# Kernel tuning notes

Hardware: AMD Instinct MI355X
Metric: run time of the kernel (lower is better)

Reference implementation:

```python
import jax, jax.numpy as jnp
import numpy as np

DIM = 768
HEADS = 12
HEAD_DIM = DIM // HEADS
HIDDEN = 4 * DIM
EPS = 1e-5
SCALE = HEAD_DIM ** -0.5


def _ln(x, g, b):
    mu = jnp.mean(x, axis=-1, keepdims=True)
    var = jnp.var(x, axis=-1, keepdims=True)
    return (x - mu) * jax.lax.rsqrt(var + EPS) * g + b


def setup_inputs() -> dict:
    key = jax.random.key(0)
    ks = jax.random.split(key, 10)
    s = lambda fan_in: 1.0 / np.sqrt(fan_in)
    return {
        "x": jax.random.normal(ks[0], (8, 4, 512, DIM), dtype=jnp.float32),
        "g1": jnp.ones((DIM,), jnp.float32),
        "b1": jnp.zeros((DIM,), jnp.float32),
        "Wqkv": jax.random.normal(ks[1], (DIM, 3 * DIM), jnp.float32) * s(DIM),
        "Wp": jax.random.normal(ks[2], (DIM, DIM), jnp.float32) * s(DIM),
        "bp": jnp.zeros((DIM,), jnp.float32),
        "g2": jnp.ones((DIM,), jnp.float32),
        "b2": jnp.zeros((DIM,), jnp.float32),
        "W1": jax.random.normal(ks[3], (DIM, HIDDEN), jnp.float32) * s(DIM),
        "bm1": jnp.zeros((HIDDEN,), jnp.float32),
        "W2": jax.random.normal(ks[4], (HIDDEN, DIM), jnp.float32) * s(HIDDEN),
        "bm2": jnp.zeros((DIM,), jnp.float32),
    }


def reference(x, g1, b1, Wqkv, Wp, bp, g2, b2, W1, bm1, W2, bm2):
    B, S, N, D = x.shape
    h = _ln(x, g1, b1)
    qkv = h @ Wqkv                                   # [B,S,N,3D]
    qkv = qkv.reshape(B, S, N, 3, HEADS, HEAD_DIM)
    q, k, v = (qkv[..., i, :, :] for i in range(3))  # [B,S,N,H,Dh]
    # scores over tokens N, per head
    attn = jnp.einsum("bsnhd,bsmhd->bshnm", q, k) * SCALE
    attn = jax.nn.softmax(attn, axis=-1)
    y = jnp.einsum("bshnm,bsmhd->bsnhd", attn, v).reshape(B, S, N, D)
    y = y @ Wp + bp
    x = x + y
    h2 = _ln(x, g2, b2)
    m = jax.nn.gelu(h2 @ W1 + bm1, approximate=False) @ W2 + bm2
    return x + m
```

## Files before the change

### kernel.cpp

```cpp
#include <hip/hip_runtime.h>
#include <hip/hip_bf16.h>
#include <cstdint>


typedef __bf16 bf16;
typedef bf16 bf16x8 __attribute__((ext_vector_type(8)));
typedef float f32x4 __attribute__((ext_vector_type(4)));
typedef uint32_t u32;

__device__ __forceinline__ f32x4 mfma16(bf16x8 a, bf16x8 b, f32x4 c){
  return __builtin_amdgcn_mfma_f32_16x16x32_bf16(a, b, c, 0, 0, 0);
}

__device__ __forceinline__ void gload16(const void* g, const void* l){
  __builtin_amdgcn_global_load_lds(
      (__attribute__((address_space(1))) u32*)(uintptr_t)g,
      (__attribute__((address_space(3))) u32*)(u32)(uintptr_t)l,
      16, 0, 0);
}

__global__ __launch_bounds__(256)
void transpose_cast(const float* __restrict__ W, bf16* __restrict__ Wt, int K, int N)
{
  __shared__ float t[64][65];
  int n0 = blockIdx.x * 64, k0 = blockIdx.y * 64;
  int tid = threadIdx.x;
  int c = tid & 63, r4 = tid >> 6;
#pragma unroll
  for (int i = 0; i < 16; ++i){
    int r = r4 * 16 + i;
    t[r][c] = W[(size_t)(k0 + r) * N + n0 + c];
  }
  __syncthreads();
#pragma unroll
  for (int i = 0; i < 16; ++i){
    int r = r4 * 16 + i;
    Wt[(size_t)(n0 + r) * K + k0 + c] = (bf16)t[c][r];
  }
}

__global__ __launch_bounds__(256)
void ln_kernel(const float* __restrict__ x, const float* __restrict__ g,
               const float* __restrict__ b, bf16* __restrict__ out)
{
  int row = blockIdx.x;
  int tid = threadIdx.x;
  const float* xr = x + (size_t)row * 768;
  float v0 = xr[tid], v1 = xr[tid + 256], v2 = xr[tid + 512];
  float s = v0 + v1 + v2;
  float ss = v0*v0 + v1*v1 + v2*v2;
#pragma unroll
  for (int m = 1; m < 64; m <<= 1){
    s  += __shfl_xor(s,  m, 64);
    ss += __shfl_xor(ss, m, 64);
  }
  __shared__ float red[8];
  int w = tid >> 6, l = tid & 63;
  if (l == 0){ red[w] = s; red[4 + w] = ss; }
  __syncthreads();
  s  = red[0] + red[1] + red[2] + red[3];
  ss = red[4] + red[5] + red[6] + red[7];
  float mu  = s * (1.0f / 768.0f);
  float var = ss * (1.0f / 768.0f) - mu * mu;
  float rs  = rsqrtf(var + 1e-5f);
  bf16* o = out + (size_t)row * 768;
  o[tid]       = (bf16)((v0 - mu) * rs * g[tid]       + b[tid]);
  o[tid + 256] = (bf16)((v1 - mu) * rs * g[tid + 256] + b[tid + 256]);
  o[tid + 512] = (bf16)((v2 - mu) * rs * g[tid + 512] + b[tid + 512]);
}

template<int EPI>
__global__ __launch_bounds__(512, 2)
void gemm256(const bf16* __restrict__ A, const bf16* __restrict__ Bt,
             const float* __restrict__ bias, const float* __restrict__ res,
             void* __restrict__ Cout, int M, int N, int K)
{
  extern __shared__ bf16 lds[];
  const int tid = threadIdx.x;
  const int w = tid >> 6, l = tid & 63;
  const int lr = l & 15, lg = l >> 4;
  const int wr = w >> 2, wc = w & 3;
  const int nbm = M >> 8, nbn = N >> 8;
  const int nwg = nbm * nbn;
  const int cpx = nwg >> 3;
  const int bid = (int)blockIdx.x;
  const int sw  = (bid & 7) * cpx + (bid >> 3);
  const int bm = sw % nbm, bn = sw / nbm;
  const int rowA0 = bm << 8, colB0 = bn << 8;

  f32x4 acc[8][4];
#pragma unroll
  for (int i = 0; i < 8; ++i)
#pragma unroll
    for (int j = 0; j < 4; ++j) acc[i][j] = f32x4{0.f, 0.f, 0.f, 0.f};

  const int srow = l >> 3;
  const int sg   = (l & 7) ^ srow;
  auto stA = [&](int T, int q){
    bf16* dst = lds + (size_t)(T & 1) * 32768 + q * 4096 + w * 512;
    int row = q * 64 + w * 8 + srow;
    gload16(A + (size_t)(rowA0 + row) * K + T * 64 + sg * 8, dst);
  };
  auto stB = [&](int T, int nh, int j){
    int hh = j * 8 + w;
    int row0 = (hh >> 2) * 64 + nh * 32 + (hh & 3) * 8;
    bf16* dst = lds + (size_t)(T & 1) * 32768 + 16384 + row0 * 64;
    int row = row0 + srow;
    gload16(Bt + (size_t)(colB0 + row) * K + T * 64 + sg * 8, dst);
  };

  const int NT = K >> 6;

  stA(0,0); stA(0,2); stB(0,0,0); stB(0,0,1);
  stA(0,1); stA(0,3); stB(0,1,0); stB(0,1,1);
  asm volatile("s_waitcnt vmcnt(4)" ::: "memory");
  __builtin_amdgcn_s_barrier();

#define PHASE(MH, NH, STAGE_STMT)                                              \
  {                                                                            \
    bf16x8 af[4][2], bfr[2][2];                                                \
    _Pragma("unroll")                                                          \
    for (int fr = 0; fr < 4; ++fr)                                             \
      _Pragma("unroll")                                                        \
      for (int kk = 0; kk < 2; ++kk){                                          \
        int row = wr * 128 + (MH) * 64 + fr * 16 + lr;                         \
        af[fr][kk] = *(const bf16x8*)&Abuf[row * 64 +                          \
                       (((kk * 4 + lg) ^ (lr & 7)) << 3)];                     \
      }                                                                        \
    _Pragma("unroll")                                                          \
    for (int fc = 0; fc < 2; ++fc)                                             \
      _Pragma("unroll")                                                        \
      for (int kk = 0; kk < 2; ++kk){                                          \
        int row = wc * 64 + (NH) * 32 + fc * 16 + lr;                          \
        bfr[fc][kk] = *(const bf16x8*)&Bbuf[row * 64 +                         \
                       (((kk * 4 + lg) ^ (lr & 7)) << 3)];                     \
      }                                                                        \
    STAGE_STMT;                                                                \
    if (more) asm volatile("s_waitcnt vmcnt(4)" ::: "memory");                 \
    else      asm volatile("s_waitcnt vmcnt(0)" ::: "memory");                 \
    __builtin_amdgcn_s_barrier();                                              \
    __builtin_amdgcn_s_setprio(1);                                             \
    _Pragma("unroll")                                                          \
    for (int fr = 0; fr < 4; ++fr)                                             \
      _Pragma("unroll")                                                        \
      for (int fc = 0; fc < 2; ++fc)                                           \
        _Pragma("unroll")                                                      \
        for (int kk = 0; kk < 2; ++kk)                                         \
          acc[(MH) * 4 + fr][(NH) * 2 + fc] =                                  \
              mfma16(af[fr][kk], bfr[fc][kk], acc[(MH) * 4 + fr][(NH) * 2 + fc]); \
    __builtin_amdgcn_s_setprio(0);                                             \
    __builtin_amdgcn_s_barrier();                                              \
  }

  for (int T = 0; T < NT; ++T){
    const bf16* Abuf = lds + (size_t)(T & 1) * 32768;
    const bf16* Bbuf = Abuf + 16384;
    const bool more = (T + 1 < NT);
    PHASE(0, 0, if (more){ stA(T+1,0); stA(T+1,2); })
    PHASE(1, 0, if (more){ stB(T+1,0,0); stB(T+1,0,1); })
    PHASE(0, 1, if (more){ stA(T+1,1); stA(T+1,3); })
    PHASE(1, 1, if (more){ stB(T+1,1,0); stB(T+1,1,1); })
  }
#undef PHASE

  const size_t crow = (size_t)rowA0 + wr * 128;
  const size_t ccol = (size_t)colB0 + wc * 64;
#pragma unroll
  for (int mi = 0; mi < 8; ++mi){
#pragma unroll
    for (int ni = 0; ni < 4; ++ni){
      size_t r0 = crow + (mi >> 2) * 64 + (mi & 3) * 16 + lg * 4;
      size_t c  = ccol + (ni >> 1) * 32 + (ni & 1) * 16 + lr;
#pragma unroll
      for (int i = 0; i < 4; ++i){
        size_t r = r0 + i;
        float v = acc[mi][ni][i];
        if (EPI == 0){
          ((bf16*)Cout)[r * (size_t)N + c] = (bf16)v;
        } else if (EPI == 1){
          v += bias[c];
          v = 0.5f * v * (1.0f + erff(v * 0.70710678118654752f));
          ((bf16*)Cout)[r * (size_t)N + c] = (bf16)v;
        } else {
          v += bias[c] + res[r * (size_t)N + c];
          ((float*)Cout)[r * (size_t)N + c] = v;
        }
      }
    }
  }
}

__global__ __launch_bounds__(256)
void attn_kernel(const bf16* __restrict__ qkv, bf16* __restrict__ y)
{
  int bid = blockIdx.x;
  int qt  = bid & 7;
  int bsh = bid >> 3;
  int h = bsh % 12;
  int R = bsh / 12;
  size_t rowbase = (size_t)R * 512;
  int tid = threadIdx.x, w = tid >> 6, l = tid & 63;
  int lr = l & 15, lg = l >> 4;

  __shared__ bf16 Kl[64 * 64];
  __shared__ bf16 Vt[64 * 64];
  __shared__ bf16 Pl[4][16 * 64];

  int q0 = qt * 64 + w * 16;
  bf16x8 qf[2];
#pragma unroll
  for (int ks = 0; ks < 2; ++ks)
    qf[ks] = *(const bf16x8*)&qkv[(rowbase + q0 + lr) * 2304 + h * 64 + ks * 32 + lg * 8];

  float mi[4], li[4];
  f32x4 oa[4];
#pragma unroll
  for (int i = 0; i < 4; ++i){ mi[i] = -1e30f; li[i] = 0.f; }
#pragma unroll
  for (int dt = 0; dt < 4; ++dt) oa[dt] = f32x4{0.f, 0.f, 0.f, 0.f};

  for (int c = 0; c < 8; ++c){
    __syncthreads();
    size_t tokbase = rowbase + c * 64;
#pragma unroll
    for (int it = 0; it < 2; ++it){
      int idx = it * 256 + tid;
      int t  = idx >> 3;
      int c8 = idx & 7;
      bf16x8 kv = *(const bf16x8*)&qkv[(tokbase + t) * 2304 + 768 + h * 64 + c8 * 8];
      *(bf16x8*)&Kl[t * 64 + ((c8 ^ (t & 7)) * 8)] = kv;
      bf16x8 vv = *(const bf16x8*)&qkv[(tokbase + t) * 2304 + 1536 + h * 64 + c8 * 8];
#pragma unroll
      for (int j = 0; j < 8; ++j){
        int d = c8 * 8 + j;
        Vt[d * 64 + (((t >> 3) ^ (d & 7)) * 8) + (t & 7)] = vv[j];
      }
    }
    __syncthreads();

    f32x4 s[4];
#pragma unroll
    for (int tt = 0; tt < 4; ++tt){
      f32x4 a = f32x4{0.f, 0.f, 0.f, 0.f};
#pragma unroll
      for (int ks = 0; ks < 2; ++ks){
        int row = tt * 16 + lr;
        int c8 = ks * 4 + lg;
        bf16x8 kf = *(const bf16x8*)&Kl[row * 64 + ((c8 ^ (row & 7)) * 8)];
        a = mfma16(qf[ks], kf, a);
      }
      s[tt] = a * 0.125f;
    }

    float pr[4][4];
#pragma unroll
    for (int i = 0; i < 4; ++i){
      float rm = fmaxf(fmaxf(s[0][i], s[1][i]), fmaxf(s[2][i], s[3][i]));
#pragma unroll
      for (int mm = 1; mm < 16; mm <<= 1) rm = fmaxf(rm, __shfl_xor(rm, mm, 64));
      float mn = fmaxf(mi[i], rm);
      float corr = __expf(mi[i] - mn);
      float rs = 0.f;
#pragma unroll
      for (int tt = 0; tt < 4; ++tt){
        float p = __expf(s[tt][i] - mn);
        pr[tt][i] = p;
        rs += p;
      }
#pragma unroll
      for (int mm = 1; mm < 16; mm <<= 1) rs += __shfl_xor(rs, mm, 64);
      li[i] = li[i] * corr + rs;
#pragma unroll
      for (int dt = 0; dt < 4; ++dt) oa[dt][i] *= corr;
      mi[i] = mn;
    }

#pragma unroll
    for (int i = 0; i < 4; ++i){
      int qr = lg * 4 + i;
#pragma unroll
      for (int tt = 0; tt < 4; ++tt){
        int tok = tt * 16 + lr;
        Pl[w][qr * 64 + (((tok >> 3) ^ (qr & 7)) * 8) + (tok & 7)] = (bf16)pr[tt][i];
      }
    }
    __syncthreads();

#pragma unroll
    for (int ks = 0; ks < 2; ++ks){
      bf16x8 pf = *(const bf16x8*)&Pl[w][lr * 64 + (((ks * 4 + lg) ^ (lr & 7)) * 8)];
#pragma unroll
      for (int dt = 0; dt < 4; ++dt){
        int row = dt * 16 + lr;
        int c8 = ks * 4 + lg;
        bf16x8 vf = *(const bf16x8*)&Vt[row * 64 + ((c8 ^ (row & 7)) * 8)];
        oa[dt] = mfma16(pf, vf, oa[dt]);
      }
    }
  }

#pragma unroll
  for (int i = 0; i < 4; ++i){
    float inv = 1.0f / li[i];
    size_t r = rowbase + q0 + lg * 4 + i;
#pragma unroll
    for (int dt = 0; dt < 4; ++dt)
      y[r * 768 + h * 64 + dt * 16 + lr] = (bf16)(oa[dt][i] * inv);
  }
}

extern "C" void kernel_launch(void* const* d_in, const int* in_sizes, int n_in,
                              void* d_out, int out_size, void* d_ws, size_t ws_size,
                              hipStream_t stream)
{
  (void)in_sizes; (void)n_in; (void)out_size; (void)ws_size;
  const float* x    = (const float*)d_in[0];
  const float* g1   = (const float*)d_in[1];
  const float* b1   = (const float*)d_in[2];
  const float* Wqkv = (const float*)d_in[3];
  const float* Wp   = (const float*)d_in[4];
  const float* bp   = (const float*)d_in[5];
  const float* g2   = (const float*)d_in[6];
  const float* b2   = (const float*)d_in[7];
  const float* W1   = (const float*)d_in[8];
  const float* bm1  = (const float*)d_in[9];
  const float* W2   = (const float*)d_in[10];
  const float* bm2  = (const float*)d_in[11];
  float* out = (float*)d_out;

  hipFuncSetAttribute((const void*)gemm256<0>, hipFuncAttributeMaxDynamicSharedMemorySize, 131072);
  hipFuncSetAttribute((const void*)gemm256<1>, hipFuncAttributeMaxDynamicSharedMemorySize, 131072);
  hipFuncSetAttribute((const void*)gemm256<2>, hipFuncAttributeMaxDynamicSharedMemorySize, 131072);

  char* ws = (char*)d_ws;
  size_t off = 0;
  auto alloc = [&](size_t nbytes) -> void* {
    void* p = ws + off;
    off += (nbytes + 255) & ~(size_t)255;
    return p;
  };
  bf16* WqkvT = (bf16*)alloc((size_t)2304 * 768 * 2);
  bf16* WpT   = (bf16*)alloc((size_t)768 * 768 * 2);
  bf16* W1T   = (bf16*)alloc((size_t)3072 * 768 * 2);
  bf16* W2T   = (bf16*)alloc((size_t)768 * 3072 * 2);
  char* R1 = (char*)alloc((size_t)16384 * 768 * 2);
  char* R2 = (char*)alloc((size_t)16384 * 3072 * 2);
  bf16* h   = (bf16*)R1;
  bf16* yb  = (bf16*)R1;
  bf16* h2  = (bf16*)R1;
  bf16* qkv = (bf16*)R2;
  bf16* m1  = (bf16*)R2;
  float* x2 = out;

  transpose_cast<<<dim3(36, 12), dim3(256), 0, stream>>>(Wqkv, WqkvT, 768, 2304);
  transpose_cast<<<dim3(12, 12), dim3(256), 0, stream>>>(Wp,   WpT,   768, 768);
  transpose_cast<<<dim3(48, 12), dim3(256), 0, stream>>>(W1,   W1T,   768, 3072);
  transpose_cast<<<dim3(12, 48), dim3(256), 0, stream>>>(W2,   W2T,   3072, 768);

  ln_kernel<<<dim3(16384), dim3(256), 0, stream>>>(x, g1, b1, h);
  gemm256<0><<<dim3(576), dim3(512), 131072, stream>>>(h, WqkvT, nullptr, nullptr,
                                                       (void*)qkv, 16384, 2304, 768);
  attn_kernel<<<dim3(3072), dim3(256), 0, stream>>>(qkv, yb);
  gemm256<2><<<dim3(192), dim3(512), 131072, stream>>>(yb, WpT, bp, x,
                                                       (void*)x2, 16384, 768, 768);
  ln_kernel<<<dim3(16384), dim3(256), 0, stream>>>(x2, g2, b2, h2);
  gemm256<1><<<dim3(768), dim3(512), 131072, stream>>>(h2, W1T, bm1, nullptr,
                                                       (void*)m1, 16384, 3072, 768);
  gemm256<2><<<dim3(192), dim3(512), 131072, stream>>>(m1, W2T, bm2, x2,
                                                       (void*)out, 16384, 768, 3072);
}
```

Baseline: 658.6 us.

## Use 128-row GEMM tiles for narrow-N projections and restructure K-loop phases

Templates the GEMM on the M-tile height so the two N=768 GEMMs (attention output projection and MLP down projection) use 128x256 tiles, doubling their workgroup count from 192 to 384 so more CUs are busy. The K-loop is rewritten to reuse A fragments across the two N halves and to keep both B halves in registers, with the staging and waitcnt sequence reorganised per tile shape. The block-to-tile mapping is also swapped to iterate N fastest. Smaller tiles lower per-block reuse and raise global traffic for those GEMMs, and the changed vmcnt accounting risks hazards if it is miscounted.

After: 686.3 us. 1.04x slower.

```diff
diff --git a/kernel.cpp b/kernel.cpp
--- a/kernel.cpp
+++ b/kernel.cpp
@@ -69,104 +69,147 @@
   o[tid + 512] = (bf16)((v2 - mu) * rs * g[tid + 512] + b[tid + 512]);
 }
 
-template<int EPI>
+template<int EPI, int BMQ>
 __global__ __launch_bounds__(512, 2)
 void gemm256(const bf16* __restrict__ A, const bf16* __restrict__ Bt,
              const float* __restrict__ bias, const float* __restrict__ res,
              void* __restrict__ Cout, int M, int N, int K)
 {
+  constexpr int BM   = BMQ * 64;
+  constexpr int MHN  = BMQ / 2;
+  constexpr int ABUF = BM * 64;
+  constexpr int BUFE = ABUF + 16384;
   extern __shared__ bf16 lds[];
   const int tid = threadIdx.x;
   const int w = tid >> 6, l = tid & 63;
   const int lr = l & 15, lg = l >> 4;
   const int wr = w >> 2, wc = w & 3;
-  const int nbm = M >> 8, nbn = N >> 8;
+  const int nbm = M / BM, nbn = N >> 8;
   const int nwg = nbm * nbn;
   const int cpx = nwg >> 3;
   const int bid = (int)blockIdx.x;
   const int sw  = (bid & 7) * cpx + (bid >> 3);
-  const int bm = sw % nbm, bn = sw / nbm;
-  const int rowA0 = bm << 8, colB0 = bn << 8;
-
-  f32x4 acc[8][4];
-#pragma unroll
-  for (int i = 0; i < 8; ++i)
+  const int bn = sw % nbn, bm = sw / nbn;
+  const int rowA0 = bm * BM, colB0 = bn << 8;
+
+  f32x4 acc[MHN * 4][4];
+#pragma unroll
+  for (int i = 0; i < MHN * 4; ++i)
 #pragma unroll
     for (int j = 0; j < 4; ++j) acc[i][j] = f32x4{0.f, 0.f, 0.f, 0.f};
 
   const int srow = l >> 3;
   const int sg   = (l & 7) ^ srow;
-  auto stA = [&](int T, int q){
-    bf16* dst = lds + (size_t)(T & 1) * 32768 + q * 4096 + w * 512;
+
+  bf16* nbuf = lds;
+  int   ktn  = 0;
+
+  auto stA = [&](int q){
+    bf16* dst = nbuf + q * 4096 + w * 512;
     int row = q * 64 + w * 8 + srow;
-    gload16(A + (size_t)(rowA0 + row) * K + T * 64 + sg * 8, dst);
+    gload16(A + (size_t)(rowA0 + row) * K + ktn + sg * 8, dst);
   };
-  auto stB = [&](int T, int nh, int j){
+  auto stB = [&](int nh, int j){
     int hh = j * 8 + w;
     int row0 = (hh >> 2) * 64 + nh * 32 + (hh & 3) * 8;
-    bf16* dst = lds + (size_t)(T & 1) * 32768 + 16384 + row0 * 64;
-    int row = row0 + srow;
-    gload16(Bt + (size_t)(colB0 + row) * K + T * 64 + sg * 8, dst);
+    bf16* dst = nbuf + ABUF + row0 * 64;
+    gload16(Bt + (size_t)(colB0 + row0 + srow) * K + ktn + sg * 8, dst);
   };
 
   const int NT = K >> 6;
 
-  stA(0,0); stA(0,2); stB(0,0,0); stB(0,0,1);
-  stA(0,1); stA(0,3); stB(0,1,0); stB(0,1,1);
-  asm volatile("s_waitcnt vmcnt(4)" ::: "memory");
+  if (BMQ == 4){
+    stA(0); stA(2); stB(0,0); stB(0,1); stB(1,0); stB(1,1); stA(1); stA(3);
+    asm volatile("s_waitcnt vmcnt(4)" ::: "memory");
+  } else {
+    stA(0); stA(1); stB(0,0); stB(0,1); stB(1,0); stB(1,1);
+    asm volatile("s_waitcnt vmcnt(2)" ::: "memory");
+  }
   __builtin_amdgcn_s_barrier();
 
-#define PHASE(MH, NH, STAGE_STMT)                                              \
-  {                                                                            \
-    bf16x8 af[4][2], bfr[2][2];                                                \
-    _Pragma("unroll")                                                          \
-    for (int fr = 0; fr < 4; ++fr)                                             \
-      _Pragma("unroll")                                                        \
-      for (int kk = 0; kk < 2; ++kk){                                          \
-        int row = wr * 128 + (MH) * 64 + fr * 16 + lr;                         \
-        af[fr][kk] = *(const bf16x8*)&Abuf[row * 64 +                          \
-                       (((kk * 4 + lg) ^ (lr & 7)) << 3)];                     \
-      }                                                                        \
-    _Pragma("unroll")                                                          \
-    for (int fc = 0; fc < 2; ++fc)                                             \
-      _Pragma("unroll")                                                        \
-      for (int kk = 0; kk < 2; ++kk){                                          \
-        int row = wc * 64 + (NH) * 32 + fc * 16 + lr;                          \
-        bfr[fc][kk] = *(const bf16x8*)&Bbuf[row * 64 +                         \
-                       (((kk * 4 + lg) ^ (lr & 7)) << 3)];                     \
-      }                                                                        \
-    STAGE_STMT;                                                                \
-    if (more) asm volatile("s_waitcnt vmcnt(4)" ::: "memory");                 \
-    else      asm volatile("s_waitcnt vmcnt(0)" ::: "memory");                 \
-    __builtin_amdgcn_s_barrier();                                              \
-    __builtin_amdgcn_s_setprio(1);                                             \
-    _Pragma("unroll")                                                          \
-    for (int fr = 0; fr < 4; ++fr)                                             \
-      _Pragma("unroll")                                                        \
-      for (int fc = 0; fc < 2; ++fc)                                           \
-        _Pragma("unroll")                                                      \
-        for (int kk = 0; kk < 2; ++kk)                                         \
-          acc[(MH) * 4 + fr][(NH) * 2 + fc] =                                  \
-              mfma16(af[fr][kk], bfr[fc][kk], acc[(MH) * 4 + fr][(NH) * 2 + fc]); \
-    __builtin_amdgcn_s_setprio(0);                                             \
-    __builtin_amdgcn_s_barrier();                                              \
-  }
+  bf16x8 af[4][2];
+  bf16x8 bfr[2][2][2];
+
+#define RDA(MH)                                                               \
+  _Pragma("unroll")                                                           \
+  for (int fr = 0; fr < 4; ++fr)                                              \
+    _Pragma("unroll")                                                         \
+    for (int kk = 0; kk < 2; ++kk){                                           \
+      int row = wr * (BM / 2) + (MH) * 64 + fr * 16 + lr;                     \
+      af[fr][kk] = *(const bf16x8*)&Abuf[row * 64 +                           \
+                     (((kk * 4 + lg) ^ (lr & 7)) << 3)];                      \
+    }
+#define RDB(NH)                                                               \
+  _Pragma("unroll")                                                           \
+  for (int fc = 0; fc < 2; ++fc)                                              \
+    _Pragma("unroll")                                                         \
+    for (int kk = 0; kk < 2; ++kk){                                           \
+      int row = wc * 64 + (NH) * 32 + fc * 16 + lr;                           \
+      bfr[NH][fc][kk] = *(const bf16x8*)&Bbuf[row * 64 +                      \
+                     (((kk * 4 + lg) ^ (lr & 7)) << 3)];                      \
+    }
+#define MM(MH, NH)                                                            \
+  __builtin_amdgcn_s_setprio(1);                                              \
+  _Pragma("unroll")                                                           \
+  for (int fr = 0; fr < 4; ++fr)                                              \
+    _Pragma("unroll")                                                         \
+    for (int fc = 0; fc < 2; ++fc)                                            \
+      _Pragma("unroll")                                                       \
+      for (int kk = 0; kk < 2; ++kk)                                          \
+        acc[(MH) * 4 + fr][(NH) * 2 + fc] =                                   \
+            mfma16(af[fr][kk], bfr[NH][fc][kk], acc[(MH) * 4 + fr][(NH) * 2 + fc]); \
+  __builtin_amdgcn_s_setprio(0);
 
   for (int T = 0; T < NT; ++T){
-    const bf16* Abuf = lds + (size_t)(T & 1) * 32768;
-    const bf16* Bbuf = Abuf + 16384;
+    const bf16* Abuf = lds + (size_t)(T & 1) * BUFE;
+    const bf16* Bbuf = Abuf + ABUF;
+    nbuf = lds + (size_t)((T + 1) & 1) * BUFE;
+    ktn  = (T + 1) << 6;
     const bool more = (T + 1 < NT);
-    PHASE(0, 0, if (more){ stA(T+1,0); stA(T+1,2); })
-    PHASE(1, 0, if (more){ stB(T+1,0,0); stB(T+1,0,1); })
-    PHASE(0, 1, if (more){ stA(T+1,1); stA(T+1,3); })
-    PHASE(1, 1, if (more){ stB(T+1,1,0); stB(T+1,1,1); })
-  }
-#undef PHASE
-
-  const size_t crow = (size_t)rowA0 + wr * 128;
+
+    RDA(0); RDB(0);
+    if (BMQ == 4){ if (more){ stA(0); stA(2); }
+                   if (more) asm volatile("s_waitcnt vmcnt(4)" ::: "memory");
+                   else      asm volatile("s_waitcnt vmcnt(0)" ::: "memory"); }
+    else         { if (more){ stA(0); stA(1); stB(0,0); }
+                   if (more) asm volatile("s_waitcnt vmcnt(3)" ::: "memory");
+                   else      asm volatile("s_waitcnt vmcnt(0)" ::: "memory"); }
+    MM(0, 0);
+    __builtin_amdgcn_s_barrier();
+
+    RDB(1);
+    if (BMQ == 4){ if (more){ stB(0,0); stB(0,1); }
+                   if (more) asm volatile("s_waitcnt vmcnt(4)" ::: "memory");
+                   else      asm volatile("s_waitcnt vmcnt(0)" ::: "memory"); }
+    else         { if (more){ stB(0,1); stB(1,0); stB(1,1); }
+                   if (more) asm volatile("s_waitcnt vmcnt(2)" ::: "memory");
+                   else      asm volatile("s_waitcnt vmcnt(0)" ::: "memory"); }
+    MM(0, 1);
+    __builtin_amdgcn_s_barrier();
+
+    if (BMQ == 4){
+      RDA(1);
+      if (more){ stB(1,0); stB(1,1); }
+      if (more) asm volatile("s_waitcnt vmcnt(4)" ::: "memory");
+      else      asm volatile("s_waitcnt vmcnt(0)" ::: "memory");
+      MM(1, 0);
+      __builtin_amdgcn_s_barrier();
+
+      if (more){ stA(1); stA(3); }
+      if (more) asm volatile("s_waitcnt vmcnt(4)" ::: "memory");
+      else      asm volatile("s_waitcnt vmcnt(0)" ::: "memory");
+      MM(1, 1);
+      __builtin_amdgcn_s_barrier();
+    }
+  }
+#undef RDA
+#undef RDB
+#undef MM
+
+  const size_t crow = (size_t)rowA0 + wr * (BM / 2);
   const size_t ccol = (size_t)colB0 + wc * 64;
 #pragma unroll
-  for (int mi = 0; mi < 8; ++mi){
+  for (int mi = 0; mi < MHN * 4; ++mi){
 #pragma unroll
     for (int ni = 0; ni < 4; ++ni){
       size_t r0 = crow + (mi >> 2) * 64 + (mi & 3) * 16 + lg * 4;
@@ -328,9 +371,9 @@
   const float* bm2  = (const float*)d_in[11];
   float* out = (float*)d_out;
 
-  hipFuncSetAttribute((const void*)gemm256<0>, hipFuncAttributeMaxDynamicSharedMemorySize, 131072);
-  hipFuncSetAttribute((const void*)gemm256<1>, hipFuncAttributeMaxDynamicSharedMemorySize, 131072);
-  hipFuncSetAttribute((const void*)gemm256<2>, hipFuncAttributeMaxDynamicSharedMemorySize, 131072);
+  hipFuncSetAttribute((const void*)gemm256<0,4>, hipFuncAttributeMaxDynamicSharedMemorySize, 131072);
+  hipFuncSetAttribute((const void*)gemm256<1,4>, hipFuncAttributeMaxDynamicSharedMemorySize, 131072);
+  hipFuncSetAttribute((const void*)gemm256<2,2>, hipFuncAttributeMaxDynamicSharedMemorySize, 98304);
 
   char* ws = (char*)d_ws;
   size_t off = 0;
@@ -358,14 +401,14 @@
   transpose_cast<<<dim3(12, 48), dim3(256), 0, stream>>>(W2,   W2T,   3072, 768);
 
   ln_kernel<<<dim3(16384), dim3(256), 0, stream>>>(x, g1, b1, h);
-  gemm256<0><<<dim3(576), dim3(512), 131072, stream>>>(h, WqkvT, nullptr, nullptr,
-                                                       (void*)qkv, 16384, 2304, 768);
+  gemm256<0,4><<<dim3(576), dim3(512), 131072, stream>>>(h, WqkvT, nullptr, nullptr,
+                                                         (void*)qkv, 16384, 2304, 768);
   attn_kernel<<<dim3(3072), dim3(256), 0, stream>>>(qkv, yb);
-  gemm256<2><<<dim3(192), dim3(512), 131072, stream>>>(yb, WpT, bp, x,
-                                                       (void*)x2, 16384, 768, 768);
+  gemm256<2,2><<<dim3(384), dim3(512), 98304, stream>>>(yb, WpT, bp, x,
+                                                        (void*)x2, 16384, 768, 768);
   ln_kernel<<<dim3(16384), dim3(256), 0, stream>>>(x2, g2, b2, h2);
-  gemm256<1><<<dim3(768), dim3(512), 131072, stream>>>(h2, W1T, bm1, nullptr,
-                                                       (void*)m1, 16384, 3072, 768);
-  gemm256<2><<<dim3(192), dim3(512), 131072, stream>>>(m1, W2T, bm2, x2,
-                                                       (void*)out, 16384, 768, 3072);
-}
+  gemm256<1,4><<<dim3(768), dim3(512), 131072, stream>>>(h2, W1T, bm1, nullptr,
+                                                         (void*)m1, 16384, 3072, 768);
+  gemm256<2,2><<<dim3(384), dim3(512), 98304, stream>>>(m1, W2T, bm2, x2,
+                                                        (void*)out, 16384, 768, 3072);
+}
```
